# Optimization experiments

Hardware: AMD Instinct MI355X
Metric: run time of the kernel (lower is better)

Reference implementation:

```python
import jax, jax.numpy as jnp
import numpy as np

B, C, N, IC = 4, 64, 4096, 32  # batch, in_channels(=g_channels), nodes, inter_channels


def setup_inputs() -> dict:
    key = jax.random.key(0)
    ks = jax.random.split(key, 8)
    s_c = (2.0 / C) ** 0.5   # kaiming-ish scales
    s_i = (2.0 / C) ** 0.5
    x = jax.random.normal(ks[0], (B, C, N), dtype=jnp.float32)
    g_w = jax.random.normal(ks[1], (C, C), dtype=jnp.float32) * s_c      # g: 1x1 conv (out=C, in=C)
    g_b = jnp.zeros((C,), dtype=jnp.float32)
    theta_w = jax.random.normal(ks[2], (IC, C), dtype=jnp.float32) * s_i  # theta: (out=IC, in=C)
    theta_b = jnp.zeros((IC,), dtype=jnp.float32)
    phi_w = jax.random.normal(ks[3], (IC, C), dtype=jnp.float32) * s_i
    phi_b = jnp.zeros((IC,), dtype=jnp.float32)
    cp_w = jax.random.normal(ks[4], (2 * IC,), dtype=jnp.float32) * (2.0 / (2 * IC)) ** 0.5  # concat_project 1x1 conv, no bias
    C_k = jnp.zeros((N, N), dtype=jnp.float32)  # learned adjacency bias, init zeros
    return {"x": x, "g_w": g_w, "g_b": g_b, "theta_w": theta_w, "theta_b": theta_b,
            "phi_w": phi_w, "phi_b": phi_b, "cp_w": cp_w, "C_k": C_k}


def reference(x, g_w, g_b, theta_w, theta_b, phi_w, phi_b, cp_w, C_k):
    # 1x1 convs are plain GEMMs over the node dim
    g_x = jnp.einsum('oc,bcn->bno', g_w, x) + g_b            # (B, N, C)
    th = jnp.einsum('oc,bcn->bon', theta_w, x) + theta_b[:, None]  # (B, IC, N)
    ph = jnp.einsum('oc,bcn->bon', phi_w, x) + phi_b[:, None]      # (B, IC, N)
    # concat_project on [theta_i ; phi_j] with a 1x1 conv is algebraically an outer sum:
    # f[b,i,j] = w_th . theta[b,:,i] + w_ph . phi[b,:,j]
    a = jnp.einsum('c,bcn->bn', cp_w[:IC], th)  # (B, N)
    p = jnp.einsum('c,bcn->bn', cp_w[IC:], ph)  # (B, N)
    f = a[:, :, None] + p[:, None, :]           # (B, N, N)
    attention = jax.nn.softmax(jax.nn.leaky_relu(f, negative_slope=0.2), axis=-1) + C_k
    y = jnp.einsum('bij,bjo->boi', attention, g_x)  # (B, C, N)
    return y
```

## Files before the change

kernel.cpp:

```cpp
#include <hip/hip_runtime.h>


#define B  4
#define C  64
#define N  4096
#define IC 32
#define NS 4104
#define NR 4097
#define MAGIC 0x13572468
#define CKQ 1048576
#define GWP 65

#define OFF_FLAG   248
#define OFF_A      256
#define OFF_P      (OFF_A + B*N)
#define OFF_Q      (OFF_P + B*N)
#define OFF_PERM   (OFF_Q + B*N)
#define OFF_PRES   (OFF_PERM + B*N)
#define OFF_SUFS   (OFF_PRES + B*NS)
#define OFF_S1     (OFF_SUFS + B*NS)
#define OFF_S2     (OFF_S1 + B*64*64)
#define OFF_GX     (OFF_S2 + B*64*64)
#define OFF_PREG   (OFF_GX + B*N*64)
#define OFF_SUFG   (OFF_PREG + B*NR*64)

#define CK_NZ(v) ((v.x != 0.f) | (v.y != 0.f) | (v.z != 0.f) | (v.w != 0.f))

__global__ __launch_bounds__(256) void k1_gx(
    const float* __restrict__ x, const float* __restrict__ g_w,
    const float* __restrict__ g_b, const float* __restrict__ theta_w,
    const float* __restrict__ theta_b, const float* __restrict__ phi_w,
    const float* __restrict__ phi_b, const float* __restrict__ cp_w,
    const float* __restrict__ Ck, float* __restrict__ ws) {
  __shared__ float gwT[GWP * C];
  __shared__ float xl[C * 32];
  __shared__ float lu[C], lv[C], cst[2];
  const int tid = threadIdx.x;
  const int b = blockIdx.x >> 7;
  const int n0 = (blockIdx.x & 127) << 5;
  const float4* c4 = (const float4*)Ck;
  float4 ck[8];
  {
    int idx = (blockIdx.x << 8) + tid;
#pragma unroll
    for (int t = 0; t < 8; ++t) { ck[t] = c4[idx]; idx += 131072; }
  }
  for (int idx = tid; idx < C * C; idx += 256) {
    int o = idx >> 6, cc = idx & 63;
    gwT[cc * GWP + o] = g_w[idx];
  }
  {
    const float4* x4 = (const float4*)x;
    float4* xl4 = (float4*)xl;
#pragma unroll
    for (int idx = tid; idx < C * 8; idx += 256) {
      int cc = idx >> 3, nn4 = idx & 7;
      xl4[cc * 8 + nn4] = x4[(size_t)((b << 6) + cc) * (N >> 2) + (n0 >> 2) + nn4];
    }
  }
  if (tid < 64) {
    float u = 0.f;
    for (int k = 0; k < IC; ++k) u += cp_w[k] * theta_w[k * C + tid];
    lu[tid] = u;
  } else if (tid < 128) {
    int c = tid - 64;
    float v = 0.f;
    for (int k = 0; k < IC; ++k) v += cp_w[IC + k] * phi_w[k * C + c];
    lv[c] = v;
  } else if (tid == 128) {
    float ca = 0.f, cp2 = 0.f;
    for (int k = 0; k < IC; ++k) { ca += cp_w[k] * theta_b[k]; cp2 += cp_w[IC + k] * phi_b[k]; }
    cst[0] = ca; cst[1] = cp2;
  }
  __syncthreads();
  if (tid < 32) {
    float au = cst[0], pu = cst[1];
    for (int cc = 0; cc < C; ++cc) {
      float xv = xl[cc * 32 + tid];
      au += lu[cc] * xv;
      pu += lv[cc] * xv;
    }
    ws[OFF_A + (b << 12) + n0 + tid] = au;
    ws[OFF_P + (b << 12) + n0 + tid] = pu;
  }
  const int o = tid & 63, g4 = tid >> 6;
  const float bb = g_b[o];
  float a0 = bb, a1 = bb, a2 = bb, a3 = bb, a4 = bb, a5 = bb, a6 = bb, a7 = bb;
  for (int cc = 0; cc < C; ++cc) {
    float gv = gwT[cc * GWP + o];
    const float4 xa = *(const float4*)&xl[cc * 32 + (g4 << 3)];
    const float4 xb = *(const float4*)&xl[cc * 32 + (g4 << 3) + 4];
    a0 += gv * xa.x; a1 += gv * xa.y; a2 += gv * xa.z; a3 += gv * xa.w;
    a4 += gv * xb.x; a5 += gv * xb.y; a6 += gv * xb.z; a7 += gv * xb.w;
  }
  float* gx = ws + OFF_GX + (size_t)((b << 12) + n0 + (g4 << 3)) * C + o;
  gx[0]   = a0; gx[64]  = a1; gx[128] = a2; gx[192] = a3;
  gx[256] = a4; gx[320] = a5; gx[384] = a6; gx[448] = a7;
  bool nz = (CK_NZ(ck[0]) | CK_NZ(ck[1])) | (CK_NZ(ck[2]) | CK_NZ(ck[3])) |
            (CK_NZ(ck[4]) | CK_NZ(ck[5])) | (CK_NZ(ck[6]) | CK_NZ(ck[7]));
  if (__any(nz) && (tid & 63) == 0)
    atomicExch((int*)ws + OFF_FLAG, MAGIC);
}

__global__ __launch_bounds__(1024) void k2_rank(const float* __restrict__ Ck,
                                                float* __restrict__ ws) {
  __shared__ float lp[N];
  __shared__ int partials[32][33];
  const int tid = threadIdx.x;
  const int b = blockIdx.x >> 7;
  const int rg = blockIdx.x & 127;
  const float4* c4 = (const float4*)Ck + CKQ;
  float4 ck0, ck1;
  {
    int idx = (blockIdx.x << 10) + tid;
    ck0 = c4[idx]; ck1 = c4[idx + 524288];
  }
  const float* p = ws + OFF_P + b * N;
  ((float4*)lp)[tid] = ((const float4*)p)[tid];
  const int row = tid & 31, chunk = tid >> 5;
  const int i = (rg << 5) + row;
  __syncthreads();
  const float my = lp[i];
  const int c0 = chunk << 7;
  const float4* lp4 = (const float4*)(lp + c0);
  int r0 = 0, r1 = 0, r2 = 0, r3 = 0;
  for (int j = 0; j < 32; ++j) {
    float4 v = lp4[j];
    int k = c0 + (j << 2);
    r0 += (v.x < my) || (v.x == my && (k + 0) < i);
    r1 += (v.y < my) || (v.y == my && (k + 1) < i);
    r2 += (v.z < my) || (v.z == my && (k + 2) < i);
    r3 += (v.w < my) || (v.w == my && (k + 3) < i);
  }
  partials[row][chunk] = (r0 + r1) + (r2 + r3);
  __syncthreads();
  if (tid < 32) {
    int rank = 0;
#pragma unroll
    for (int c = 0; c < 32; ++c) rank += partials[tid][c];
    const int ii = (rg << 5) + tid;
    ws[OFF_Q + (b << 12) + rank] = lp[ii];
    ((int*)ws)[OFF_PERM + (b << 12) + rank] = ii;
  }
  bool nz = CK_NZ(ck0) | CK_NZ(ck1);
  if (__any(nz) && (tid & 63) == 0)
    atomicExch((int*)ws + OFF_FLAG, MAGIC);
}

__global__ __launch_bounds__(1024) void k34_scan_prefix(const float* __restrict__ Ck,
                                                        float* __restrict__ ws) {
  __shared__ float sA[1024], sB[1024];
  const int tid = threadIdx.x;
  const int bid = blockIdx.x;
  const float4* c4 = (const float4*)Ck + 2 * CKQ;
  float4 ck[8];
#pragma unroll
  for (int t = 0; t < 8; ++t) ck[t] = make_float4(0.f, 0.f, 0.f, 0.f);
  {
    int idx = (bid << 10) + tid;
#pragma unroll
    for (int t = 0; t < 8; ++t) {
      if (idx < 2 * CKQ) ck[t] = c4[idx];
      idx += 266240;
    }
  }
  if (bid < B) {
    const int b = bid;
    float* wt2 = sA;
    float* wt1 = sA + 16;
    float* wo2 = sA + 32;
    float* wo1 = sA + 49;
    const float* q = ws + OFF_Q + b * N;
    const float4 qv4 = ((const float4*)q)[tid];
    float e1r[4], e2r[4];
    e2r[0] = expf(0.2f * qv4.x); e1r[0] = expf(qv4.x);
    e2r[1] = expf(0.2f * qv4.y); e1r[1] = expf(qv4.y);
    e2r[2] = expf(0.2f * qv4.z); e1r[2] = expf(qv4.z);
    e2r[3] = expf(0.2f * qv4.w); e1r[3] = expf(qv4.w);
    float s2 = e2r[0] + e2r[1] + e2r[2] + e2r[3];
    float s1 = e1r[0] + e1r[1] + e1r[2] + e1r[3];
    const int lane = tid & 63, wave = tid >> 6;
    float x2 = s2, x1 = s1;
    for (int off = 1; off < 64; off <<= 1) {
      float t2 = __shfl_up(x2, off, 64);
      float t1 = __shfl_up(x1, off, 64);
      if (lane >= off) { x2 += t2; x1 += t1; }
    }
    if (lane == 63) { wt2[wave] = x2; wt1[wave] = x1; }
    __syncthreads();
    if (wave == 0 && lane < 17) {
      float a2 = 0.f, a1 = 0.f;
      for (int w = 0; w < 16; ++w) {
        if (w < lane) { a2 += wt2[w]; a1 += wt1[w]; }
      }
      wo2[lane] = a2; wo1[lane] = a1;
    }
    __syncthreads();
    const float excl2 = wo2[wave] + (x2 - s2);
    const float incl1 = wo1[wave] + x1;
    const float tot1 = wo1[16];
    float* PreS = ws + OFF_PRES + b * NS;
    float* SufS = ws + OFF_SUFS + b * NS;
    const int base = tid << 2;
    float run = excl2;
#pragma unroll
    for (int j = 0; j < 4; ++j) { PreS[base + j] = run; run += e2r[j]; }
    if (tid == 1023) PreS[N] = run;
    run = tot1 - incl1;
#pragma unroll
    for (int j = 3; j >= 0; --j) { run += e1r[j]; SufS[base + j] = run; }
    if (tid == 1023) SufS[N] = 0.f;
  } else {
    const int b2 = bid - B;
    const int b = b2 >> 6, c = b2 & 63;
    const int o = tid & 63, kk = tid >> 6;
    const float* q = ws + OFF_Q + b * N;
    const int* perm = (const int*)ws + OFF_PERM + b * N;
    const float* gx = ws + OFF_GX + ((size_t)b << 18);
    float* PreG = ws + OFF_PREG + (size_t)b * NR * 64;
    float* SufG = ws + OFF_SUFG + (size_t)b * NR * 64;
    const int k0 = (c << 6) + (kk << 2);
    float w1[4], w2[4];
    float p1 = 0.f, p2 = 0.f;
#pragma unroll
    for (int r = 0; r < 4; ++r) {
      float qq = q[k0 + r];
      float gg = gx[((size_t)perm[k0 + r] << 6) + o];
      w1[r] = expf(qq) * gg;
      w2[r] = expf(0.2f * qq) * gg;
      p1 += w1[r]; p2 += w2[r];
    }
    sA[(kk << 6) + o] = p2;
    sB[(kk << 6) + o] = p1;
    __syncthreads();
    if (tid < 64) {
      float t2 = 0.f, t1 = 0.f;
#pragma unroll
      for (int g = 0; g < 16; ++g) { t2 += sA[(g << 6) + o]; t1 += sB[(g << 6) + o]; }
      ws[OFF_S2 + (size_t)(((b << 6) + c) << 6) + o] = t2;
      ws[OFF_S1 + (size_t)(((b << 6) + c) << 6) + o] = t1;
    }
    float offp = 0.f, offs = 0.f;
    for (int kp = 0; kp < kk; ++kp) offp += sA[(kp << 6) + o];
    for (int kp = kk + 1; kp < 16; ++kp) offs += sB[(kp << 6) + o];
    float run = offp;
#pragma unroll
    for (int r = 0; r < 4; ++r) { PreG[(size_t)(k0 + r) * 64 + o] = run; run += w2[r]; }
    run = offs;
#pragma unroll
    for (int r = 3; r >= 0; --r) { run += w1[r]; SufG[(size_t)(k0 + r) * 64 + o] = run; }
  }
  bool nz = (CK_NZ(ck[0]) | CK_NZ(ck[1])) | (CK_NZ(ck[2]) | CK_NZ(ck[3])) |
            (CK_NZ(ck[4]) | CK_NZ(ck[5])) | (CK_NZ(ck[6]) | CK_NZ(ck[7]));
  if (__any(nz) && (tid & 63) == 0)
    atomicExch((int*)ws + OFF_FLAG, MAGIC);
}

__global__ __launch_bounds__(1024) void k5_out(const float* __restrict__ Ck,
                                               float* __restrict__ ws,
                                               float* __restrict__ y) {
  __shared__ float lq[N];
  __shared__ float cum2[65 * 64];
  __shared__ float suf1[65 * 64];
  __shared__ float part1[1024], part2[1024];
  const int tid = threadIdx.x;
  const int b = blockIdx.x >> 6, rg = blockIdx.x & 63;
  ((float4*)lq)[tid]   = ((const float4*)(ws + OFF_Q + (b << 12)))[tid];
  ((float4*)cum2)[tid] = ((const float4*)(ws + OFF_S2 + ((size_t)b << 12)))[tid];
  ((float4*)suf1)[tid] = ((const float4*)(ws + OFF_S1 + ((size_t)b << 12)))[tid];
  if (tid < 64) suf1[(64 << 6) + tid] = 0.f;
  __syncthreads();
  const int o = tid & 63, g = tid >> 6;
  const int cg0 = g << 2;
  const float q0 = cum2[(cg0 << 6) + o],       q1 = cum2[((cg0 + 1) << 6) + o],
              q2 = cum2[((cg0 + 2) << 6) + o], q3 = cum2[((cg0 + 3) << 6) + o];
  const float s0 = suf1[(cg0 << 6) + o],       s1v = suf1[((cg0 + 1) << 6) + o],
              s2v = suf1[((cg0 + 2) << 6) + o], s3 = suf1[((cg0 + 3) << 6) + o];
  part2[(g << 6) + o] = (q0 + q1) + (q2 + q3);
  part1[(g << 6) + o] = (s0 + s1v) + (s2v + s3);
  __syncthreads();
  {
    float base2 = 0.f, base1 = 0.f;
    for (int gg = 0; gg < g; ++gg) base2 += part2[(gg << 6) + o];
    for (int gg = g + 1; gg < 16; ++gg) base1 += part1[(gg << 6) + o];
    float run = base2;
    cum2[(cg0 << 6) + o] = run; run += q0;
    cum2[((cg0 + 1) << 6) + o] = run; run += q1;
    cum2[((cg0 + 2) << 6) + o] = run; run += q2;
    cum2[((cg0 + 3) << 6) + o] = run; run += q3;
    if (g == 15) cum2[(64 << 6) + o] = run;
    run = base1;
    suf1[((cg0 + 3) << 6) + o] = run; run += s3;
    suf1[((cg0 + 2) << 6) + o] = run; run += s2v;
    suf1[((cg0 + 1) << 6) + o] = run; run += s1v;
    suf1[(cg0 << 6) + o] = run;
  }
  const int io = tid & 63, og = tid >> 6;
  const int i = (rg << 6) + io;
  float ai = ws[OFF_A + (b << 12) + i];
  float thr = -ai;
  int lo = 0, hi = N;
  while (lo < hi) { int m = (lo + hi) >> 1; if (lq[m] <= thr) lo = m + 1; else hi = m; }
  const int k = lo;
  const int kc = k >> 6;
  float e1 = expf(ai), e2 = expf(0.2f * ai);
  float den = e1 * ws[OFF_SUFS + b * NS + k] + e2 * ws[OFF_PRES + b * NS + k];
  float inv = 1.0f / den;
  float4 pl = {0.f, 0.f, 0.f, 0.f}, sl = pl;
  if (k < N) {
    pl = ((const float4*)(ws + OFF_PREG + ((size_t)b * NR + k) * 64))[og];
    sl = ((const float4*)(ws + OFF_SUFG + ((size_t)b * NR + k) * 64))[og];
  }
  __syncthreads();
  float4 c2  = ((const float4*)(cum2 + (kc << 6)))[og];
  float4 s1g = ((const float4*)(suf1 + (kc << 6)))[og];
  float* yb = y + ((size_t)((b << 6) + (og << 2))) * N + i;
  yb[0]             = (e1 * (s1g.x + sl.x) + e2 * (c2.x + pl.x)) * inv;
  yb[(size_t)N]     = (e1 * (s1g.y + sl.y) + e2 * (c2.y + pl.y)) * inv;
  yb[(size_t)2 * N] = (e1 * (s1g.z + sl.z) + e2 * (c2.z + pl.z)) * inv;
  yb[(size_t)3 * N] = (e1 * (s1g.w + sl.w) + e2 * (c2.w + pl.w)) * inv;
  if (((const volatile int*)ws)[OFF_FLAG] == MAGIC) {
    __syncthreads();
    const int it = rg;
    const int oo = tid & 63, jj = tid >> 6;
    const float* gx = ws + OFF_GX + ((size_t)b << 18);
    float (*red)[64] = (float(*)[64])lq;
    for (int ii = 0; ii < 64; ++ii) {
      int irow = (it << 6) + ii;
      float acc = 0.f;
      for (int j = jj; j < N; j += 16)
        acc += Ck[(size_t)irow * N + j] * gx[((size_t)j << 6) + oo];
      red[jj][oo] = acc;
      __syncthreads();
      if (jj == 0) {
        float s = 0.f;
#pragma unroll
        for (int g2 = 0; g2 < 16; ++g2) s += red[g2][oo];
        y[((size_t)((b << 6) + oo)) * N + irow] += s;
      }
      __syncthreads();
    }
  }
}

extern "C" void kernel_launch(void* const* d_in, const int* in_sizes, int n_in,
                              void* d_out, int out_size, void* d_ws, size_t ws_size,
                              hipStream_t stream) {
  (void)in_sizes; (void)n_in; (void)out_size; (void)ws_size;
  const float* x       = (const float*)d_in[0];
  const float* g_w     = (const float*)d_in[1];
  const float* g_b     = (const float*)d_in[2];
  const float* theta_w = (const float*)d_in[3];
  const float* theta_b = (const float*)d_in[4];
  const float* phi_w   = (const float*)d_in[5];
  const float* phi_b   = (const float*)d_in[6];
  const float* cp_w    = (const float*)d_in[7];
  const float* Ck      = (const float*)d_in[8];
  float* ws = (float*)d_ws;
  float* y  = (float*)d_out;

  hipLaunchKernelGGL(k1_gx, dim3(512), dim3(256), 0, stream,
                     x, g_w, g_b, theta_w, theta_b, phi_w, phi_b, cp_w, Ck, ws);
  hipLaunchKernelGGL(k2_rank, dim3(512), dim3(1024), 0, stream, Ck, ws);
  hipLaunchKernelGGL(k34_scan_prefix, dim3(B + B * 64), dim3(1024), 0, stream, Ck, ws);
  hipLaunchKernelGGL(k5_out, dim3(B * 64), dim3(1024), 0, stream, Ck, ws, y);
}
```

Before: 143.5 us.

## Halve k1 grid with 64-node tiles and rebalance C_k scan across kernels

k1 now handles 64 nodes per block, so it launches half as many blocks, and each thread computes two output channels for eight nodes, which reuses each x load across more FMAs. The scan of the C_k matrix for nonzero entries is redistributed: k1 and k2 read more of it and k34 reads less, with new offsets that still cover the whole matrix. The goal is fewer blocks in k1 and less redundant g_w staging, plus shorter C_k loads in k34. The cost is more registers per thread in k1 and a longer critical path in k1 and k2.

```diff
diff --git a/kernel.cpp b/kernel.cpp
--- a/kernel.cpp
+++ b/kernel.cpp
@@ -8,8 +8,11 @@
 #define NS 4104
 #define NR 4097
 #define MAGIC 0x13572468
-#define CKQ 1048576
 #define GWP 65
+
+#define CK_K2_BASE  1048576
+#define CK_K34_BASE 2621440
+#define CK_K34_LEN  1572864
 
 #define OFF_FLAG   248
 #define OFF_A      256
@@ -33,17 +36,17 @@
     const float* __restrict__ phi_b, const float* __restrict__ cp_w,
     const float* __restrict__ Ck, float* __restrict__ ws) {
   __shared__ float gwT[GWP * C];
-  __shared__ float xl[C * 32];
+  __shared__ float xl[C * 64];
   __shared__ float lu[C], lv[C], cst[2];
   const int tid = threadIdx.x;
-  const int b = blockIdx.x >> 7;
-  const int n0 = (blockIdx.x & 127) << 5;
+  const int b = blockIdx.x >> 6;
+  const int n0 = (blockIdx.x & 63) << 6;
   const float4* c4 = (const float4*)Ck;
   float4 ck[8];
   {
     int idx = (blockIdx.x << 8) + tid;
 #pragma unroll
-    for (int t = 0; t < 8; ++t) { ck[t] = c4[idx]; idx += 131072; }
+    for (int t = 0; t < 8; ++t) { ck[t] = c4[idx]; idx += 65536; }
   }
   for (int idx = tid; idx < C * C; idx += 256) {
     int o = idx >> 6, cc = idx & 63;
@@ -53,9 +56,9 @@
     const float4* x4 = (const float4*)x;
     float4* xl4 = (float4*)xl;
 #pragma unroll
-    for (int idx = tid; idx < C * 8; idx += 256) {
-      int cc = idx >> 3, nn4 = idx & 7;
-      xl4[cc * 8 + nn4] = x4[(size_t)((b << 6) + cc) * (N >> 2) + (n0 >> 2) + nn4];
+    for (int idx = tid; idx < C * 16; idx += 256) {
+      int cc = idx >> 4, nn4 = idx & 15;
+      xl4[cc * 16 + nn4] = x4[(size_t)((b << 6) + cc) * (N >> 2) + (n0 >> 2) + nn4];
     }
   }
   if (tid < 64) {
@@ -73,31 +76,46 @@
     cst[0] = ca; cst[1] = cp2;
   }
   __syncthreads();
-  if (tid < 32) {
+  bool nz = (CK_NZ(ck[0]) | CK_NZ(ck[1])) | (CK_NZ(ck[2]) | CK_NZ(ck[3])) |
+            (CK_NZ(ck[4]) | CK_NZ(ck[5])) | (CK_NZ(ck[6]) | CK_NZ(ck[7]));
+  {
+    int idx = (blockIdx.x << 8) + tid + 524288;
+#pragma unroll
+    for (int t = 0; t < 8; ++t) { ck[t] = c4[idx]; idx += 65536; }
+  }
+  if (tid < 64) {
     float au = cst[0], pu = cst[1];
     for (int cc = 0; cc < C; ++cc) {
-      float xv = xl[cc * 32 + tid];
+      float xv = xl[cc * 64 + tid];
       au += lu[cc] * xv;
       pu += lv[cc] * xv;
     }
     ws[OFF_A + (b << 12) + n0 + tid] = au;
     ws[OFF_P + (b << 12) + n0 + tid] = pu;
   }
-  const int o = tid & 63, g4 = tid >> 6;
-  const float bb = g_b[o];
-  float a0 = bb, a1 = bb, a2 = bb, a3 = bb, a4 = bb, a5 = bb, a6 = bb, a7 = bb;
+  const int o = tid & 31, g8 = tid >> 5;
+  const float bb0 = g_b[o], bb1 = g_b[o + 32];
+  float a0[8], a1[8];
+#pragma unroll
+  for (int j = 0; j < 8; ++j) { a0[j] = bb0; a1[j] = bb1; }
   for (int cc = 0; cc < C; ++cc) {
-    float gv = gwT[cc * GWP + o];
-    const float4 xa = *(const float4*)&xl[cc * 32 + (g4 << 3)];
-    const float4 xb = *(const float4*)&xl[cc * 32 + (g4 << 3) + 4];
-    a0 += gv * xa.x; a1 += gv * xa.y; a2 += gv * xa.z; a3 += gv * xa.w;
-    a4 += gv * xb.x; a5 += gv * xb.y; a6 += gv * xb.z; a7 += gv * xb.w;
-  }
-  float* gx = ws + OFF_GX + (size_t)((b << 12) + n0 + (g4 << 3)) * C + o;
-  gx[0]   = a0; gx[64]  = a1; gx[128] = a2; gx[192] = a3;
-  gx[256] = a4; gx[320] = a5; gx[384] = a6; gx[448] = a7;
-  bool nz = (CK_NZ(ck[0]) | CK_NZ(ck[1])) | (CK_NZ(ck[2]) | CK_NZ(ck[3])) |
-            (CK_NZ(ck[4]) | CK_NZ(ck[5])) | (CK_NZ(ck[6]) | CK_NZ(ck[7]));
+    const float gv0 = gwT[cc * GWP + o];
+    const float gv1 = gwT[cc * GWP + o + 32];
+    const float4 xa = *(const float4*)&xl[cc * 64 + (g8 << 3)];
+    const float4 xb = *(const float4*)&xl[cc * 64 + (g8 << 3) + 4];
+    a0[0] += gv0 * xa.x; a0[1] += gv0 * xa.y; a0[2] += gv0 * xa.z; a0[3] += gv0 * xa.w;
+    a0[4] += gv0 * xb.x; a0[5] += gv0 * xb.y; a0[6] += gv0 * xb.z; a0[7] += gv0 * xb.w;
+    a1[0] += gv1 * xa.x; a1[1] += gv1 * xa.y; a1[2] += gv1 * xa.z; a1[3] += gv1 * xa.w;
+    a1[4] += gv1 * xb.x; a1[5] += gv1 * xb.y; a1[6] += gv1 * xb.z; a1[7] += gv1 * xb.w;
+  }
+  float* gx = ws + OFF_GX + (size_t)((b << 12) + n0 + (g8 << 3)) * C + o;
+#pragma unroll
+  for (int j = 0; j < 8; ++j) {
+    gx[j * 64]      = a0[j];
+    gx[j * 64 + 32] = a1[j];
+  }
+  nz |= (CK_NZ(ck[0]) | CK_NZ(ck[1])) | (CK_NZ(ck[2]) | CK_NZ(ck[3])) |
+        (CK_NZ(ck[4]) | CK_NZ(ck[5])) | (CK_NZ(ck[6]) | CK_NZ(ck[7]));
   if (__any(nz) && (tid & 63) == 0)
     atomicExch((int*)ws + OFF_FLAG, MAGIC);
 }
@@ -109,11 +127,11 @@
   const int tid = threadIdx.x;
   const int b = blockIdx.x >> 7;
   const int rg = blockIdx.x & 127;
-  const float4* c4 = (const float4*)Ck + CKQ;
-  float4 ck0, ck1;
+  const float4* c4 = (const float4*)Ck + CK_K2_BASE;
+  float4 ck0, ck1, ck2;
   {
     int idx = (blockIdx.x << 10) + tid;
-    ck0 = c4[idx]; ck1 = c4[idx + 524288];
+    ck0 = c4[idx]; ck1 = c4[idx + 524288]; ck2 = c4[idx + 1048576];
   }
   const float* p = ws + OFF_P + b * N;
   ((float4*)lp)[tid] = ((const float4*)p)[tid];
@@ -142,7 +160,7 @@
     ws[OFF_Q + (b << 12) + rank] = lp[ii];
     ((int*)ws)[OFF_PERM + (b << 12) + rank] = ii;
   }
-  bool nz = CK_NZ(ck0) | CK_NZ(ck1);
+  bool nz = CK_NZ(ck0) | CK_NZ(ck1) | CK_NZ(ck2);
   if (__any(nz) && (tid & 63) == 0)
     atomicExch((int*)ws + OFF_FLAG, MAGIC);
 }
@@ -152,15 +170,15 @@
   __shared__ float sA[1024], sB[1024];
   const int tid = threadIdx.x;
   const int bid = blockIdx.x;
-  const float4* c4 = (const float4*)Ck + 2 * CKQ;
-  float4 ck[8];
-#pragma unroll
-  for (int t = 0; t < 8; ++t) ck[t] = make_float4(0.f, 0.f, 0.f, 0.f);
+  const float4* c4 = (const float4*)Ck + CK_K34_BASE;
+  float4 ck[6];
+#pragma unroll
+  for (int t = 0; t < 6; ++t) ck[t] = make_float4(0.f, 0.f, 0.f, 0.f);
   {
     int idx = (bid << 10) + tid;
 #pragma unroll
-    for (int t = 0; t < 8; ++t) {
-      if (idx < 2 * CKQ) ck[t] = c4[idx];
+    for (int t = 0; t < 6; ++t) {
+      if (idx < CK_K34_LEN) ck[t] = c4[idx];
       idx += 266240;
     }
   }
@@ -251,7 +269,7 @@
     for (int r = 3; r >= 0; --r) { run += w1[r]; SufG[(size_t)(k0 + r) * 64 + o] = run; }
   }
   bool nz = (CK_NZ(ck[0]) | CK_NZ(ck[1])) | (CK_NZ(ck[2]) | CK_NZ(ck[3])) |
-            (CK_NZ(ck[4]) | CK_NZ(ck[5])) | (CK_NZ(ck[6]) | CK_NZ(ck[7]));
+            (CK_NZ(ck[4]) | CK_NZ(ck[5]));
   if (__any(nz) && (tid & 63) == 0)
     atomicExch((int*)ws + OFF_FLAG, MAGIC);
 }
@@ -359,7 +377,7 @@
   float* ws = (float*)d_ws;
   float* y  = (float*)d_out;
 
-  hipLaunchKernelGGL(k1_gx, dim3(512), dim3(256), 0, stream,
+  hipLaunchKernelGGL(k1_gx, dim3(256), dim3(256), 0, stream,
                      x, g_w, g_b, theta_w, theta_b, phi_w, phi_b, cp_w, Ck, ws);
   hipLaunchKernelGGL(k2_rank, dim3(512), dim3(1024), 0, stream, Ck, ws);
   hipLaunchKernelGGL(k34_scan_prefix, dim3(B + B * 64), dim3(1024), 0, stream, Ck, ws);
```

Result: no change. 141.5 us (-1.3%).
